# Kernel tuning notes

Measured on AMD Instinct MI355X. Metric: run time of the kernel, lower is better.

## Reference

```python
import jax, jax.numpy as jnp
import numpy as np


def setup_inputs() -> dict:
    key = jax.random.key(0)
    k1, k2 = jax.random.split(key)
    B, T, F = 8, 1000, 257
    m = jax.random.normal(k1, (B, 27, T, F), dtype=jnp.float32)
    x = jax.random.normal(k2, (B, F, T, 2), dtype=jnp.float32)
    return {"m": m, "x": x}


def reference(m, x):
    # m: (B, 27, T, F) real; x: (B, F, T, 2) real (re/im stacked)
    B, _, T, F = m.shape
    SQ3_2 = float(np.sqrt(3.0) / 2.0)
    v = jnp.array([1.0 + 0.0j, -0.5 + 1j * SQ3_2, -0.5 - 1j * SQ3_2],
                  dtype=jnp.complex64)  # complex basis, shape (3,)
    # (b, 3, 9, t, f) -> contract basis axis -> complex (b, 9, t, f)
    mr = m.reshape(B, 3, 9, T, F).astype(jnp.complex64)
    H = jnp.einsum('r,brctf->bctf', v, mr)
    M = H.reshape(B, 3, 3, T, F)  # per-pixel 3x3 complex mask

    # complex spectrogram (B, T, F); original permutes (B,F,T,2)->(B,2,T,F)
    xc = (x[..., 0] + 1j * x[..., 1]).transpose(0, 2, 1)
    # ZeroPad2d([1,1,2,0]) on (T,F): top=2 (causal time), left=right=1 (freq)
    xp = jnp.pad(xc, ((0, 0), (2, 0), (1, 1)))

    # Fused stencil: accumulate 3x3 complex MAC without materializing unfold
    x_enh = jnp.zeros((B, T, F), dtype=jnp.complex64)
    for mm in range(3):
        for nn in range(3):
            x_enh = x_enh + M[:, mm, nn] * xp[:, mm:mm + T, nn:nn + F]

    # (B,T,F) complex -> (B,T,F,2) -> (B,F,T,2)
    out = jnp.stack([x_enh.real, x_enh.imag], axis=-1).transpose(0, 2, 1, 3)
    return out
```

## Files before the change

### kernel.cpp

```cpp
#include <hip/hip_runtime.h>

#define B_  8
#define T_  1000
#define F_  257
#define SQ3_2 0.8660254037844386f

__global__ __launch_bounds__(512)
void ccm_fused(const float* __restrict__ m, const float2* __restrict__ x,
               float2* __restrict__ out) {
    __shared__ float2 xls[10 * 66];
    __shared__ float2 stage[8][66];

    const int b   = blockIdx.z;
    const int f0  = blockIdx.x * 64;
    const int t0  = blockIdx.y * 8;
    const int tid = threadIdx.x;
    const int lf  = tid & 63;
    const int lt  = tid >> 6;
    const int f   = f0 + lf;
    const int t   = t0 + lt;

    const float2* xb = x + (size_t)b * F_ * T_;
    #pragma unroll
    for (int pass = 0; pass < 2; ++pass) {
        const int idx = tid + pass * 512;
        if (idx < 660) {
            const int j = idx / 10;
            const int r = idx - j * 10;
            const int tt = t0 + r - 2;
            const int ff = f0 + j - 1;
            float2 v = make_float2(0.f, 0.f);
            if (tt >= 0 && tt < T_ && ff >= 0 && ff < F_)
                v = xb[(size_t)ff * T_ + tt];
            xls[r * 66 + j] = v;
        }
    }
    __syncthreads();

    float accr = 0.f, acci = 0.f;

    if (f < F_) {
        const float* mb = m + ((size_t)b * 27 * T_ + t) * F_ + f;
        #pragma unroll
        for (int c = 0; c < 9; ++c) {
            const float m0 = mb[(size_t)(c)      * (T_ * F_)];
            const float m1 = mb[(size_t)(c + 9)  * (T_ * F_)];
            const float m2 = mb[(size_t)(c + 18) * (T_ * F_)];
            const float hr = m0 - 0.5f * (m1 + m2);
            const float hi = SQ3_2 * (m1 - m2);
            const float2 xv = xls[(lt + c / 3) * 66 + (lf + c % 3)];
            accr = fmaf(hr, xv.x, accr);
            accr = fmaf(-hi, xv.y, accr);
            acci = fmaf(hr, xv.y, acci);
            acci = fmaf(hi, xv.x, acci);
        }
    }

    stage[lt][lf] = make_float2(accr, acci);
    __syncthreads();

    const int wf = tid >> 3;
    const int wt = tid & 7;
    if (f0 + wf < F_)
        out[(size_t)(b * F_ + f0 + wf) * T_ + (t0 + wt)] = stage[wt][wf];
}

extern "C" void kernel_launch(void* const* d_in, const int* in_sizes, int n_in,
                              void* d_out, int out_size, void* d_ws, size_t ws_size,
                              hipStream_t stream) {
    const float*  m = (const float*)d_in[0];
    const float2* x = (const float2*)d_in[1];
    float2* out = (float2*)d_out;

    dim3 mb(512);
    dim3 mg((F_ + 63) / 64, T_ / 8, B_);
    ccm_fused<<<mg, mb, 0, stream>>>(m, x, out);
}
```

Baseline: 319.6 us.

## Flatten pixel indexing and vectorize mask loads with float4 per thread

```diff
diff --git a/kernel.cpp b/kernel.cpp
--- a/kernel.cpp
+++ b/kernel.cpp
@@ -3,66 +3,104 @@
 #define B_  8
 #define T_  1000
 #define F_  257
+#define P_  (T_ * F_)
 #define SQ3_2 0.8660254037844386f
 
-__global__ __launch_bounds__(512)
+#define THREADS 512
+#define VEC     4
+#define CHUNK   (THREADS * VEC)
+#define NBLK    ((P_ + CHUNK - 1) / CHUNK)
+#define XROWS   11
+#define XCOLS   (F_ + 2)
+#define OROWS   9
+
+__global__ __launch_bounds__(THREADS)
 void ccm_fused(const float* __restrict__ m, const float2* __restrict__ x,
                float2* __restrict__ out) {
-    __shared__ float2 xls[10 * 66];
-    __shared__ float2 stage[8][66];
+    __shared__ float2 buf[XROWS * XCOLS];
 
-    const int b   = blockIdx.z;
-    const int f0  = blockIdx.x * 64;
-    const int t0  = blockIdx.y * 8;
-    const int tid = threadIdx.x;
-    const int lf  = tid & 63;
-    const int lt  = tid >> 6;
-    const int f   = f0 + lf;
-    const int t   = t0 + lt;
+    const int b      = blockIdx.z;
+    const int s      = blockIdx.x * CHUNK;
+    const int send   = min(s + CHUNK, P_);
+    const int t_lo   = s / F_;
+    const int t_base = t_lo - 2;
+    const int tid    = threadIdx.x;
 
-    const float2* xb = x + (size_t)b * F_ * T_;
-    #pragma unroll
-    for (int pass = 0; pass < 2; ++pass) {
-        const int idx = tid + pass * 512;
-        if (idx < 660) {
-            const int j = idx / 10;
-            const int r = idx - j * 10;
-            const int tt = t0 + r - 2;
-            const int ff = f0 + j - 1;
-            float2 v = make_float2(0.f, 0.f);
-            if (tt >= 0 && tt < T_ && ff >= 0 && ff < F_)
-                v = xb[(size_t)ff * T_ + tt];
-            xls[r * 66 + j] = v;
-        }
+    const float2* xb = x + (size_t)b * (F_ * T_);
+    for (int idx = tid; idx < XROWS * XCOLS; idx += THREADS) {
+        const int j  = idx / XROWS;
+        const int r  = idx - j * XROWS;
+        const int tt = t_base + r;
+        const int ff = j - 1;
+        float2 v = make_float2(0.f, 0.f);
+        if (tt >= 0 && tt < T_ && ff >= 0 && ff < F_)
+            v = xb[(size_t)ff * T_ + tt];
+        buf[r * XCOLS + j] = v;
     }
     __syncthreads();
 
-    float accr = 0.f, acci = 0.f;
+    const int  p0     = s + tid * VEC;
+    const bool active = p0 < P_;
 
-    if (f < F_) {
-        const float* mb = m + ((size_t)b * 27 * T_ + t) * F_ + f;
+    float accr[VEC], acci[VEC];
+    int   te[VEC], fe[VEC], base[VEC];
+    #pragma unroll
+    for (int e = 0; e < VEC; ++e) { accr[e] = 0.f; acci[e] = 0.f; te[e] = 0; fe[e] = 0; }
+
+    if (active) {
+        te[0] = p0 / F_;
+        fe[0] = p0 - te[0] * F_;
+        #pragma unroll
+        for (int e = 1; e < VEC; ++e) {
+            te[e] = te[e - 1];
+            fe[e] = fe[e - 1] + 1;
+            if (fe[e] == F_) { fe[e] = 0; ++te[e]; }
+        }
+        #pragma unroll
+        for (int e = 0; e < VEC; ++e)
+            base[e] = (te[e] - t_lo) * XCOLS + fe[e];
+
+        const float* mb = m + (size_t)b * 27 * P_ + p0;
         #pragma unroll
         for (int c = 0; c < 9; ++c) {
-            const float m0 = mb[(size_t)(c)      * (T_ * F_)];
-            const float m1 = mb[(size_t)(c + 9)  * (T_ * F_)];
-            const float m2 = mb[(size_t)(c + 18) * (T_ * F_)];
-            const float hr = m0 - 0.5f * (m1 + m2);
-            const float hi = SQ3_2 * (m1 - m2);
-            const float2 xv = xls[(lt + c / 3) * 66 + (lf + c % 3)];
-            accr = fmaf(hr, xv.x, accr);
-            accr = fmaf(-hi, xv.y, accr);
-            acci = fmaf(hr, xv.y, acci);
-            acci = fmaf(hi, xv.x, acci);
+            const float4 m0 = *(const float4*)(mb + (size_t)(c)      * P_);
+            const float4 m1 = *(const float4*)(mb + (size_t)(c + 9)  * P_);
+            const float4 m2 = *(const float4*)(mb + (size_t)(c + 18) * P_);
+            const int off = (c / 3) * XCOLS + (c % 3);
+            const float* f0v = (const float*)&m0;
+            const float* f1v = (const float*)&m1;
+            const float* f2v = (const float*)&m2;
+            #pragma unroll
+            for (int e = 0; e < VEC; ++e) {
+                const float  hr = f0v[e] - 0.5f * (f1v[e] + f2v[e]);
+                const float  hi = SQ3_2 * (f1v[e] - f2v[e]);
+                const float2 xv = buf[base[e] + off];
+                accr[e] = fmaf(hr,  xv.x, accr[e]);
+                accr[e] = fmaf(-hi, xv.y, accr[e]);
+                acci[e] = fmaf(hr,  xv.y, acci[e]);
+                acci[e] = fmaf(hi,  xv.x, acci[e]);
+            }
         }
     }
 
-    stage[lt][lf] = make_float2(accr, acci);
     __syncthreads();
 
-    const int wf = tid >> 3;
-    const int wt = tid & 7;
-    if (f0 + wf < F_)
-        out[(size_t)(b * F_ + f0 + wf) * T_ + (t0 + wt)] = stage[wt][wf];
+    if (active) {
+        #pragma unroll
+        for (int e = 0; e < VEC; ++e)
+            buf[(te[e] - t_lo) * F_ + fe[e]] = make_float2(accr[e], acci[e]);
+    }
+    __syncthreads();
+
+    float2* ob = out + (size_t)b * (F_ * T_);
+    for (int idx = tid; idx < OROWS * F_; idx += THREADS) {
+        const int f = idx / OROWS;
+        const int r = idx - f * OROWS;
+        const int t = t_lo + r;
+        const int p = t * F_ + f;
+        if (p >= s && p < send)
+            ob[(size_t)f * T_ + t] = buf[r * F_ + f];
+    }
 }
 
 extern "C" void kernel_launch(void* const* d_in, const int* in_sizes, int n_in,
@@ -72,7 +110,7 @@
     const float2* x = (const float2*)d_in[1];
     float2* out = (float2*)d_out;
 
-    dim3 mb(512);
-    dim3 mg((F_ + 63) / 64, T_ / 8, B_);
+    dim3 mb(THREADS);
+    dim3 mg(NBLK, 1, B_);
     ccm_fused<<<mg, mb, 0, stream>>>(m, x, out);
 }
```

Measured after the change: 333.5 us. 4.3% more time.
